# Kernel optimization log

Hardware: AMD Instinct MI355X
Metric: run time of the kernel (lower is better)

## Reference

```python
import jax, jax.numpy as jnp
import numpy as np

N, E = 100000, 1600000
IN_CH, HID, HEADS, OUT_CH = 128, 32, 2, 40
NEG_SLOPE = 0.2
BN_EPS = 1e-5


def _param(key, shape, scale=0.1):
    return scale * jax.random.normal(key, shape, dtype=jnp.float32)


def setup_inputs() -> dict:
    key = jax.random.key(0)
    ks = jax.random.split(key, 24)
    x = jax.random.normal(ks[0], (N, IN_CH), dtype=jnp.float32)
    edge_index = jax.random.randint(ks[1], (2, E), 0, N, dtype=jnp.int32)
    d0 = HEADS * HID  # 64
    inp = {
        'x': x, 'edge_index': edge_index,
        # conv0: in 128 -> 32 per head, concat -> 64
        'W0': _param(ks[2], (IN_CH, HEADS * HID)),
        'as0': _param(ks[3], (HEADS, HID)), 'ad0': _param(ks[4], (HEADS, HID)),
        'b0': jnp.zeros((d0,), jnp.float32),
        'g0': jnp.ones((d0,), jnp.float32), 'bt0': jnp.zeros((d0,), jnp.float32),
        # conv1: 64 -> 32 per head, concat -> 64
        'W1': _param(ks[5], (d0, HEADS * HID)),
        'as1': _param(ks[6], (HEADS, HID)), 'ad1': _param(ks[7], (HEADS, HID)),
        'b1': jnp.zeros((d0,), jnp.float32),
        'g1': jnp.ones((d0,), jnp.float32), 'bt1': jnp.zeros((d0,), jnp.float32),
        # conv2: 64 -> 40 per head, mean over heads -> 40
        'W2': _param(ks[8], (d0, HEADS * OUT_CH)),
        'as2': _param(ks[9], (HEADS, OUT_CH)), 'ad2': _param(ks[10], (HEADS, OUT_CH)),
        'b2': jnp.zeros((OUT_CH,), jnp.float32),
    }
    return inp


def gat_conv(x, src, dst, W, a_src, a_dst, bias, out_ch, concat):
    n = x.shape[0]
    h = (x @ W).reshape(n, HEADS, out_ch)            # [N,H,C]
    alpha_src = jnp.sum(h * a_src, axis=-1)          # [N,H]
    alpha_dst = jnp.sum(h * a_dst, axis=-1)          # [N,H]
    e = jax.nn.leaky_relu(alpha_src[src] + alpha_dst[dst], NEG_SLOPE)  # [E,H]
    # softmax over incoming edges per destination node (self loops guarantee >=1 edge)
    m = jax.ops.segment_max(e, dst, num_segments=n)
    e = jnp.exp(e - m[dst])
    s = jax.ops.segment_sum(e, dst, num_segments=n)
    alpha = e / s[dst]                                # [E,H]
    msg = h[src] * alpha[:, :, None]                  # [E,H,C]
    out = jax.ops.segment_sum(msg, dst, num_segments=n)  # [N,H,C]
    out = out.reshape(n, HEADS * out_ch) if concat else out.mean(axis=1)
    return out + bias


def batch_norm(x, gamma, beta):
    mu = jnp.mean(x, axis=0)
    var = jnp.mean(jnp.square(x - mu), axis=0)
    return gamma * (x - mu) * jax.lax.rsqrt(var + BN_EPS) + beta


def reference(x, edge_index, W0, as0, ad0, b0, g0, bt0,
              W1, as1, ad1, b1, g1, bt1, W2, as2, ad2, b2):
    n = x.shape[0]
    loops = jnp.arange(n, dtype=edge_index.dtype)
    src = jnp.concatenate([edge_index[0], loops])
    dst = jnp.concatenate([edge_index[1], loops])
    h = gat_conv(x, src, dst, W0, as0, ad0, b0, HID, True)
    h = jax.nn.elu(batch_norm(h, g0, bt0))
    h = gat_conv(h, src, dst, W1, as1, ad1, b1, HID, True)
    h = jax.nn.elu(batch_norm(h, g1, bt1))
    return gat_conv(h, src, dst, W2, as2, ad2, b2, OUT_CH, False)
```

## Files before the change

kernel.cpp:

```cpp
#include <hip/hip_runtime.h>
#include <hip/hip_bf16.h>
#include <math.h>


#define NNODES 100000
#define NEDGES 1600000
#define ENTOT  (NEDGES + NNODES)
#define NEG_SLOPE 0.2f
#define BN_EPS 1e-5f

#define NRANGE 8
#define RSIZE  (NNODES/NRANGE)
#define BCAP   262144
#define PBLK   2048
#define NB2    32

typedef unsigned short u16;
typedef unsigned int u32;
typedef unsigned long long u64;
typedef __attribute__((ext_vector_type(8))) short short8;
typedef __attribute__((ext_vector_type(4))) float f32x4;

__device__ __forceinline__ float b2f(u16 u){ union{u32 i; float f;} v; v.i=((u32)u)<<16; return v.f; }
__device__ __forceinline__ float blo(u32 u){ union{u32 i; float f;} v; v.i=u<<16; return v.f; }
__device__ __forceinline__ float bhi(u32 u){ union{u32 i; float f;} v; v.i=u&0xffff0000u; return v.f; }
__device__ __forceinline__ u16 f2b(float x){ __hip_bfloat16 b=__float2bfloat16(x); return *(u16*)&b; }
__device__ __forceinline__ float ldf(const void* p, int i, int f){
  return f ? ((const float*)p)[i] : b2f(((const u16*)p)[i]);
}

__global__ void k_detect(const u16* __restrict__ x, int* __restrict__ flag){
  __shared__ int bad;
  if(threadIdx.x==0) bad=0;
  __syncthreads();
  int cnt=0;
  for(int i=threadIdx.x;i<4096;i+=256){
    u16 v = x[2*i];
    int ex = (v>>7)&0xff;
    if(ex==0xff || (ex==0 && (v&0x7fff)!=0)) cnt++;
  }
  atomicAdd(&bad,cnt);
  __syncthreads();
  if(threadIdx.x==0) flag[0] = (bad>4)?1:0;
}

__global__ __launch_bounds__(256) void k_part2(
    const int* __restrict__ ei, int* __restrict__ gptr, u32* __restrict__ bkt){
  __shared__ int lcnt[NRANGE], gbase[NRANGE];
  int t=threadIdx.x;
  if(t<NRANGE) lcnt[t]=0;
  __syncthreads();
  const int CH=(ENTOT+PBLK-1)/PBLK;
  int beg=blockIdx.x*CH, end=beg+CH; if(end>ENTOT) end=ENTOT;
  int nd[4], ns[4], nr[4], ne=0;
  for(int i=beg+t; i<end; i+=256){
    int d=(i<NEDGES)? ei[NEDGES+i] : (i-NEDGES);
    int s=(i<NEDGES)? ei[i] : d;
    nd[ne]=d; ns[ne]=s; ne++;
  }
  #pragma unroll 4
  for(int k=0;k<ne;k++) nr[k]=atomicAdd(&lcnt[nd[k]/RSIZE],1);
  __syncthreads();
  if(t<NRANGE) gbase[t]=atomicAdd(&gptr[t],lcnt[t]);
  __syncthreads();
  #pragma unroll 4
  for(int k=0;k<ne;k++){
    int r=nd[k]/RSIZE;
    u32 e = ((u32)(nd[k]-r*RSIZE)<<17) | (u32)ns[k];
    __builtin_nontemporal_store(e, &bkt[(size_t)r*BCAP + gbase[r] + nr[k]]);
  }
}

__global__ __launch_bounds__(256) void k_hist4(
    const u32* __restrict__ bkt, const int* __restrict__ gptr, int* __restrict__ lhist){
  __shared__ int lh[RSIZE];
  int t=threadIdx.x;
  for(int i=t;i<RSIZE;i+=256) lh[i]=0;
  __syncthreads();
  int r = blockIdx.x & (NRANGE-1);
  int c = blockIdx.x >> 3;
  int n = gptr[r];
  int per=(n+NB2-1)/NB2;
  int beg=c*per, end=beg+per; if(end>n) end=n;
  const u32* bp = bkt + (size_t)r*BCAP;
  for(int i=beg+t;i<end;i+=256) atomicAdd(&lh[bp[i]>>17],1);
  __syncthreads();
  int* out = lhist + (size_t)(r*NB2+c)*RSIZE;
  for(int i=t;i<RSIZE;i+=256) out[i]=lh[i];
}

__global__ __launch_bounds__(256) void k_sumscan(int* __restrict__ lhist, int* __restrict__ cnt){
  int n = blockIdx.x*256 + threadIdx.x;
  if(n>=NNODES) return;
  int r = n/RSIZE, i = n - r*RSIZE;
  int* base = lhist + (size_t)r*NB2*RSIZE + i;
  int run=0;
  #pragma unroll 8
  for(int c=0;c<NB2;c++){
    int v = base[(size_t)c*RSIZE];
    base[(size_t)c*RSIZE] = run;
    run += v;
  }
  cnt[n]=run;
}

#define SCAN_M (NNODES+1)
#define SCAN_NB ((SCAN_M + 2047)/2048)

__global__ void k_scan_a(const int* __restrict__ cnt, int* __restrict__ bsum){
  __shared__ int red[256];
  int b=blockIdx.x, t=threadIdx.x;
  int base = b*2048 + t*8;
  int s=0;
  #pragma unroll
  for(int j=0;j<8;j++){ int idx=base+j; s += (idx<NNODES)? cnt[idx]:0; }
  red[t]=s; __syncthreads();
  for(int o=128;o>0;o>>=1){ if(t<o) red[t]+=red[t+o]; __syncthreads(); }
  if(t==0) bsum[b]=red[0];
}

__global__ void k_scan_b(int* bsum){
  if(threadIdx.x==0){
    int run=0;
    for(int i=0;i<SCAN_NB;i++){ int v=bsum[i]; bsum[i]=run; run+=v; }
  }
}

__global__ void k_scan_c(const int* __restrict__ cnt, const int* __restrict__ bsum,
                         int* __restrict__ row_ptr){
  __shared__ int lds[256];
  int b=blockIdx.x, t=threadIdx.x;
  int base=b*2048+t*8;
  int v[8]; int s=0;
  #pragma unroll
  for(int j=0;j<8;j++){ int idx=base+j; int x=(idx<NNODES)?cnt[idx]:0; v[j]=s; s+=x; }
  lds[t]=s; __syncthreads();
  for(int o=1;o<256;o<<=1){
    int other=0; if(t>=o) other=lds[t-o];
    __syncthreads();
    lds[t]+=other;
    __syncthreads();
  }
  int texcl = lds[t] - s;
  int off0 = bsum[b] + texcl;
  #pragma unroll
  for(int j=0;j<8;j++){ int idx=base+j; if(idx<SCAN_M) row_ptr[idx]=off0+v[j]; }
}

__global__ __launch_bounds__(256) void k_scatter4(
    const u32* __restrict__ bkt, const int* __restrict__ gptr,
    const int* __restrict__ row_ptr, const int* __restrict__ lhist,
    int* __restrict__ col){
  __shared__ int lofs[RSIZE];
  int t=threadIdx.x;
  int r = blockIdx.x & (NRANGE-1);
  int c = blockIdx.x >> 3;
  int lo = r*RSIZE;
  const int* cb = lhist + (size_t)(r*NB2+c)*RSIZE;
  for(int i=t;i<RSIZE;i+=256) lofs[i] = row_ptr[lo+i] + cb[i];
  __syncthreads();
  int n = gptr[r];
  int per=(n+NB2-1)/NB2;
  int beg=c*per, end=beg+per; if(end>n) end=n;
  const u32* bp = bkt + (size_t)r*BCAP;
  for(int i=beg+t;i<end;i+=256){
    u32 e=bp[i];
    int pos=atomicAdd(&lofs[e>>17],1);
    col[pos]=(int)(e & 0x1FFFF);
  }
}

template<int K, int OUTC, int HID, bool XEXT, bool BN>
__global__ __launch_bounds__(256) void k_gemm_mfma(
    const void* __restrict__ xin, const void* __restrict__ W,
    const void* __restrict__ avs, const void* __restrict__ avd,
    const float2* __restrict__ bnab,
    u16* __restrict__ hout, float* __restrict__ asrc, float* __restrict__ adst,
    const int* __restrict__ flagp)
{
  const int f = flagp[0];
  constexpr int KP = K+8;
  constexpr int RS = OUTC+8;
  constexpr int NT = OUTC/16;
  constexpr int KQ = K/32;
  __shared__ __align__(16) u16 WT[OUTC*KP];
  __shared__ __align__(16) u16 HROW[4*16*RS];
  __shared__ float AVb[2*OUTC];
  __shared__ float2 BB[K];
  int t=threadIdx.x;
  const u16* Wu=(const u16*)W; const float* Wf=(const float*)W;
  for(int i8=t*8; i8<K*OUTC; i8+=256*8){
    int k=i8/OUTC, c0=i8-k*OUTC;
    u16 w8[8];
    if(f){
      const float* wp=Wf+i8;
      float4 a=*(const float4*)wp, b=*(const float4*)(wp+4);
      w8[0]=f2b(a.x);w8[1]=f2b(a.y);w8[2]=f2b(a.z);w8[3]=f2b(a.w);
      w8[4]=f2b(b.x);w8[5]=f2b(b.y);w8[6]=f2b(b.z);w8[7]=f2b(b.w);
    } else {
      uint4 q=*(const uint4*)(Wu+i8);
      w8[0]=q.x&0xffff;w8[1]=q.x>>16;w8[2]=q.y&0xffff;w8[3]=q.y>>16;
      w8[4]=q.z&0xffff;w8[5]=q.z>>16;w8[6]=q.w&0xffff;w8[7]=q.w>>16;
    }
    #pragma unroll
    for(int u=0;u<8;u++) WT[(c0+u)*KP + k] = w8[u];
  }
  for(int idx=t; idx<2*OUTC; idx+=256)
    AVb[idx] = (idx<OUTC)? ldf(avs,idx,f) : ldf(avd,idx-OUTC,f);
  if(BN) for(int idx=t; idx<K; idx+=256) BB[idx]=bnab[idx];
  __syncthreads();

  int wv=t>>6, lane=t&63;
  int m=lane&15, quad=lane>>4;
  int grow0 = blockIdx.x*64 + wv*16;
  int growA = grow0 + m;
  bool avalid = growA < NNODES;
  int growC = avalid ? growA : 0;

  f32x4 acc[NT] = {};
  #pragma unroll
  for(int kq=0;kq<KQ;kq++){
    int k0 = kq*32 + quad*8;
    union{ u32 u[4]; short8 s8; } A;
    if(XEXT && f==1){
      const float* xr=(const float*)xin + (size_t)growC*K + k0;
      float4 p=*(const float4*)xr, q=*(const float4*)(xr+4);
      A.u[0]=f2b(p.x)|((u32)f2b(p.y)<<16);
      A.u[1]=f2b(p.z)|((u32)f2b(p.w)<<16);
      A.u[2]=f2b(q.x)|((u32)f2b(q.y)<<16);
      A.u[3]=f2b(q.z)|((u32)f2b(q.w)<<16);
    } else {
      uint4 q=*(const uint4*)((const u16*)xin + (size_t)growC*K + k0);
      A.u[0]=q.x; A.u[1]=q.y; A.u[2]=q.z; A.u[3]=q.w;
    }
    if(BN){
      #pragma unroll
      for(int j=0;j<4;j++){
        float lo=b2f(A.u[j]&0xffff), hi=b2f(A.u[j]>>16);
        float2 c1=BB[k0+2*j], c2=BB[k0+2*j+1];
        lo=c1.x*lo+c1.y; lo = lo>0.f? lo : __expf(lo)-1.f;
        hi=c2.x*hi+c2.y; hi = hi>0.f? hi : __expf(hi)-1.f;
        A.u[j]=f2b(lo)|((u32)f2b(hi)<<16);
      }
    }
    #pragma unroll
    for(int nt=0;nt<NT;nt++){
      union{ uint4 q; short8 s8; } Bf;
      Bf.q = *(const uint4*)&WT[(nt*16+m)*KP + k0];
      acc[nt] = __builtin_amdgcn_mfma_f32_16x16x32_bf16(A.s8, Bf.s8, acc[nt], 0,0,0);
    }
  }
  u16* hr = &HROW[wv*16*RS];
  #pragma unroll
  for(int nt=0;nt<NT;nt++){
    #pragma unroll
    for(int reg=0;reg<4;reg++)
      hr[(quad*4+reg)*RS + nt*16+m] = f2b(acc[nt][reg]);
  }
  __syncthreads();
  {
    int row=lane&15, task=quad, head=task&1, sd=task>>1;
    float p=0.f;
    const u16* hrow=&hr[row*RS + head*HID];
    const float* av=&AVb[sd*OUTC + head*HID];
    #pragma unroll 8
    for(int c=0;c<HID;c++) p += b2f(hrow[c])*av[c];
    int grow=grow0+row;
    if(grow<NNODES){ (sd? adst:asrc)[grow*2+head]=p; }
  }
  {
    constexpr int CH8 = OUTC/8;
    for(int idx=lane; idx<16*CH8; idx+=64){
      int rr=idx/CH8, c8=idx-rr*CH8;
      int grow=grow0+rr;
      if(grow<NNODES)
        *(uint4*)(hout + (size_t)grow*OUTC + c8*8) = *(const uint4*)&hr[rr*RS + c8*8];
    }
  }
}

template<int OUTC, bool FINAL>
__global__ __launch_bounds__(256) void k_aggf(
  const int* __restrict__ row_ptr, const int* __restrict__ col,
  const u16* __restrict__ hin, const float* __restrict__ asrcf,
  const float2* __restrict__ adst2, const void* __restrict__ bias,
  u16* __restrict__ houtb, void* __restrict__ outv, const int* __restrict__ flagp)
{
  const int f = flagp[0];
  __shared__ float vbuf[FINAL?32:1][84];
  int t = threadIdx.x;
  int g  = t>>3;
  int cg = t&7;
  int rr = blockIdx.x & 7, jb = blockIdx.x >> 3;
  int lim = RSIZE - jb*32;
  bool ok = g < lim;
  int d = rr*RSIZE + jb*32 + g;
  int base=0, deg=0;
  float2 adv = make_float2(0.f,0.f);
  if(ok){
    base = row_ptr[d];
    deg  = row_ptr[d+1] - base;
    adv  = adst2[d];
  }
  const int* cp  = col + base;
  const u16* hcg = hin + cg*8;
  float acc[8]={0,0,0,0,0,0,0,0};

  if(!FINAL){
    int ho = (cg>=4)?1:0;
    float aown = ho ? adv.y : adv.x;
    float s=0.f;
    for(int j=0;j<deg;j+=2){
      int c0 = cp[j];
      bool v1 = (j+1)<deg;
      int c1 = cp[v1 ? j+1 : j];
      float sa = asrcf[c0*2+ho];
      float sb = asrcf[c1*2+ho];
      uint4 h0 = *(const uint4*)(hcg + (size_t)c0*OUTC);
      uint4 h1 = *(const uint4*)(hcg + (size_t)c1*OUTC);
      float e0 = sa+aown; e0 = fmaxf(e0, NEG_SLOPE*e0); e0 = fminf(e0,60.f);
      float e1 = sb+aown; e1 = fmaxf(e1, NEG_SLOPE*e1); e1 = fminf(e1,60.f);
      float p0 = __expf(e0), p1 = __expf(e1);
      if(!v1) p1 = 0.f;
      s += p0 + p1;
      acc[0] += p0*blo(h0.x) + p1*blo(h1.x);
      acc[1] += p0*bhi(h0.x) + p1*bhi(h1.x);
      acc[2] += p0*blo(h0.y) + p1*blo(h1.y);
      acc[3] += p0*bhi(h0.y) + p1*bhi(h1.y);
      acc[4] += p0*blo(h0.z) + p1*blo(h1.z);
      acc[5] += p0*bhi(h0.z) + p1*bhi(h1.z);
      acc[6] += p0*blo(h0.w) + p1*blo(h1.w);
      acc[7] += p0*bhi(h0.w) + p1*bhi(h1.w);
    }
    float inv = s>0.f ? 1.f/s : 0.f;
    if(ok){
      u16 o8[8];
      #pragma unroll
      for(int k=0;k<8;k++) o8[k]=f2b(acc[k]*inv + ldf(bias,cg*8+k,f));
      uint4 ov;
      ov.x=(u32)o8[0]|((u32)o8[1]<<16); ov.y=(u32)o8[2]|((u32)o8[3]<<16);
      ov.z=(u32)o8[4]|((u32)o8[5]<<16); ov.w=(u32)o8[6]|((u32)o8[7]<<16);
      *(uint4*)(houtb + (size_t)d*64 + cg*8) = ov;
    }
  } else {
    const float2* asrc2 = (const float2*)asrcf;
    const u16* hxg = hin + 64 + cg*2;
    float accx0=0.f, accx1=0.f;
    float s0=0.f, s1=0.f;
    for(int j=0;j<deg;j+=2){
      int c0 = cp[j];
      bool v1 = (j+1)<deg;
      int c1 = cp[v1 ? j+1 : j];
      float2 sa = asrc2[c0];
      float2 sv = asrc2[c1];
      const u16* hp0 = hcg + (size_t)c0*OUTC;
      const u16* hp1 = hcg + (size_t)c1*OUTC;
      uint4 h0 = *(const uint4*)hp0;
      uint4 h1 = *(const uint4*)hp1;
      float e0 = sa.x+adv.x; e0 = fmaxf(e0, NEG_SLOPE*e0); e0 = fminf(e0,60.f);
      float e1 = sa.y+adv.y; e1 = fmaxf(e1, NEG_SLOPE*e1); e1 = fminf(e1,60.f);
      float p0 = __expf(e0), p1 = __expf(e1);
      float q0 = sv.x+adv.x; q0 = fmaxf(q0, NEG_SLOPE*q0); q0 = fminf(q0,60.f);
      float q1 = sv.y+adv.y; q1 = fmaxf(q1, NEG_SLOPE*q1); q1 = fminf(q1,60.f);
      float r0 = __expf(q0), r1 = __expf(q1);
      if(!v1){ r0=0.f; r1=0.f; }
      s0 += p0 + r0; s1 += p1 + r1;
      float pa = (cg<5)? p0 : p1;
      float pb = (cg<5)? r0 : r1;
      acc[0] += pa*blo(h0.x) + pb*blo(h1.x);
      acc[1] += pa*bhi(h0.x) + pb*bhi(h1.x);
      acc[2] += pa*blo(h0.y) + pb*blo(h1.y);
      acc[3] += pa*bhi(h0.y) + pb*bhi(h1.y);
      acc[4] += pa*blo(h0.z) + pb*blo(h1.z);
      acc[5] += pa*bhi(h0.z) + pb*bhi(h1.z);
      acc[6] += pa*blo(h0.w) + pb*blo(h1.w);
      acc[7] += pa*bhi(h0.w) + pb*bhi(h1.w);
      ushort2 ha = *(const ushort2*)(hxg + (size_t)c0*OUTC);
      ushort2 hb = *(const ushort2*)(hxg + (size_t)c1*OUTC);
      accx0 += p1*b2f(ha.x) + r1*b2f(hb.x);
      accx1 += p1*b2f(ha.y) + r1*b2f(hb.y);
    }
    float inv0 = s0>0.f?1.f/s0:0.f, inv1 = s1>0.f?1.f/s1:0.f;
    if(ok){
      #pragma unroll
      for(int k=0;k<8;k++)
        vbuf[g][cg*8+k] = acc[k]*((cg<5)?inv0:inv1);
      vbuf[g][64+cg*2]   = accx0*inv1;
      vbuf[g][64+cg*2+1] = accx1*inv1;
    }
    __syncthreads();
    for(int idx=t; idx<32*40; idx+=256){
      int gg=idx/40, ch=idx-gg*40;
      if(gg<lim){
        int dd = rr*RSIZE + jb*32 + gg;
        float res = 0.5f*(vbuf[gg][ch] + vbuf[gg][40+ch]) + ldf(bias,ch,f);
        if(f) ((float*)outv)[(size_t)dd*40+ch] = res;
        else  ((__hip_bfloat16*)outv)[(size_t)dd*40+ch] = __float2bfloat16(res);
      }
    }
  }
}

__global__ __launch_bounds__(256) void k_bnstats(const u16* __restrict__ h, float* __restrict__ stats){
  __shared__ float red[4][128];
  int t=threadIdx.x; int c=t&63; int g=t>>6;
  float s=0.f,q=0.f;
  for(int r=blockIdx.x*4+g; r<NNODES; r+=gridDim.x*4){
    float v=b2f(h[(size_t)r*64+c]); s+=v; q+=v*v;
  }
  red[g][c]=s; red[g][64+c]=q;
  __syncthreads();
  if(t<128){
    float tot=red[0][t]+red[1][t]+red[2][t]+red[3][t];
    atomicAdd(&stats[t], tot);
  }
}

__global__ void k_bnfinal(const float* __restrict__ stats,
                          const void* __restrict__ gm, const void* __restrict__ bt,
                          float2* __restrict__ bnab, const int* __restrict__ flagp){
  const int f = flagp[0];
  int c=threadIdx.x;
  if(c>=64) return;
  float mu=stats[c]*(1.0f/NNODES);
  float var=stats[64+c]*(1.0f/NNODES)-mu*mu;
  var = var>0.f?var:0.f;
  float A = ldf(gm,c,f)*rsqrtf(var+BN_EPS);
  float B = ldf(bt,c,f) - A*mu;
  bnab[c]=make_float2(A,B);
}

extern "C" void kernel_launch(void* const* d_in, const int* in_sizes, int n_in,
                              void* d_out, int out_size, void* d_ws, size_t ws_size,
                              hipStream_t stream){
  const void* x  =d_in[0];
  const int* ei =(const int*)d_in[1];
  const void* W0 =d_in[2];  const void* as0=d_in[3];  const void* ad0=d_in[4];
  const void* b0 =d_in[5];  const void* g0 =d_in[6];  const void* bt0=d_in[7];
  const void* W1 =d_in[8];  const void* as1=d_in[9];  const void* ad1=d_in[10];
  const void* b1 =d_in[11]; const void* g1 =d_in[12]; const void* bt1=d_in[13];
  const void* W2 =d_in[14]; const void* as2=d_in[15]; const void* ad2=d_in[16];
  const void* b2 =d_in[17];

  char* ws=(char*)d_ws;
  size_t off=0;
  auto alloc=[&](size_t bytes)->void*{ void* p=ws+off; off+=(bytes+255)&~(size_t)255; return p; };
  int*    flag   =(int*)   alloc(256);
  int*    row_ptr=(int*)   alloc((size_t)(NNODES+1)*4);
  int*    cnt    =(int*)   alloc((size_t)NNODES*4);
  int*    colx   =(int*)   alloc((size_t)ENTOT*4);
  int*    bsum   =(int*)   alloc((size_t)SCAN_NB*4);
  int*    gptr   =(int*)   alloc(256);
  u32*    bkt    =(u32*)   alloc((size_t)NRANGE*BCAP*4);
  u16*    hA     =(u16*)   alloc((size_t)100032*80*2);
  u16*    hB0    =(u16*)   alloc((size_t)100032*64*2);
  u16*    hB1    =(u16*)   alloc((size_t)100032*64*2);
  float*  asrc   =(float*) alloc((size_t)NNODES*2*4);
  float*  adst   =(float*) alloc((size_t)NNODES*2*4);
  float*  stats  =(float*) alloc(128*4);
  float2* bnab   =(float2*)alloc(64*8);
  int*    lhist  =(int*)hA;

  k_detect<<<1,256,0,stream>>>((const u16*)x, flag);

  (void)hipMemsetAsync(gptr,0,256,stream);
  k_part2  <<<PBLK,256,0,stream>>>(ei,gptr,bkt);
  k_hist4  <<<NRANGE*NB2,256,0,stream>>>(bkt,gptr,lhist);
  k_sumscan<<<(NNODES+255)/256,256,0,stream>>>(lhist,cnt);
  k_scan_a <<<SCAN_NB,256,0,stream>>>(cnt,bsum);
  k_scan_b <<<1,64,0,stream>>>(bsum);
  k_scan_c <<<SCAN_NB,256,0,stream>>>(cnt,bsum,row_ptr);
  k_scatter4<<<NRANGE*NB2,256,0,stream>>>(bkt,gptr,row_ptr,lhist,colx);

  int gG = (NNODES+63)/64;
  int gA = NRANGE * ((RSIZE + 31)/32);
  k_gemm_mfma<128,64,32,true ,false><<<gG,256,0,stream>>>(
      x,W0,as0,ad0,nullptr,hA,asrc,adst,flag);
  k_aggf<64,false><<<gA,256,0,stream>>>(row_ptr,colx,hA,
      asrc,(const float2*)adst,b0,hB0,nullptr,flag);
  (void)hipMemsetAsync(stats,0,512,stream);
  k_bnstats<<<256,256,0,stream>>>(hB0,stats);
  k_bnfinal<<<1,64,0,stream>>>(stats,g0,bt0,bnab,flag);
  k_gemm_mfma<64,64,32,false,true ><<<gG,256,0,stream>>>(
      hB0,W1,as1,ad1,bnab,hA,asrc,adst,flag);
  k_aggf<64,false><<<gA,256,0,stream>>>(row_ptr,colx,hA,
      asrc,(const float2*)adst,b1,hB1,nullptr,flag);
  (void)hipMemsetAsync(stats,0,512,stream);
  k_bnstats<<<256,256,0,stream>>>(hB1,stats);
  k_bnfinal<<<1,64,0,stream>>>(stats,g1,bt1,bnab,flag);
  k_gemm_mfma<64,80,40,false,true ><<<gG,256,0,stream>>>(
      hB1,W2,as2,ad2,bnab,hA,asrc,adst,flag);
  k_aggf<80,true ><<<gA,256,0,stream>>>(row_ptr,colx,hA,
      asrc,(const float2*)adst,b2,nullptr,d_out,flag);

  (void)in_sizes;(void)n_in;(void)out_size;(void)ws_size;
}
```

Baseline: 447.1 us.

## Bucket edges by source range and add phased block sync in aggregation

CSR construction now splits edges into buckets keyed by both destination range and source sub-band, with a local LDS sort before writing each bucket. Within each destination, columns then come out grouped by source band, which should improve cache locality of the gathers in aggregation. The aggregation loops are also cut into four phases with a __syncthreads between them, so warps in a block walk through source bands together and reuse L2. The cost is extra LDS work and scans in partitioning, plus block barriers that can stall warps on high-degree rows. Bucket capacity is now fixed at 24576 entries, which holds only for roughly uniform random graphs.

```diff
diff --git a/kernel.cpp b/kernel.cpp
--- a/kernel.cpp
+++ b/kernel.cpp
@@ -11,11 +11,16 @@
 
 #define NRANGE 8
 #define RSIZE  (NNODES/NRANGE)
-#define BCAP   262144
-#define PBLK   2048
-#define NB2    32
+#define SB     16
+#define SBS    (NNODES/SB)
+#define NBKT   (SB*NRANGE)
+#define BCAP   24576
+#define PBLK2  512
+#define CH2    ((ENTOT+PBLK2-1)/PBLK2)
+#define CHP    3328
 
 typedef unsigned short u16;
+typedef unsigned char u8;
 typedef unsigned int u32;
 typedef unsigned long long u64;
 typedef __attribute__((ext_vector_type(8))) short short8;
@@ -44,30 +49,55 @@
   if(threadIdx.x==0) flag[0] = (bad>4)?1:0;
 }
 
-__global__ __launch_bounds__(256) void k_part2(
+__global__ __launch_bounds__(256) void k_part3(
     const int* __restrict__ ei, int* __restrict__ gptr, u32* __restrict__ bkt){
-  __shared__ int lcnt[NRANGE], gbase[NRANGE];
+  __shared__ u32 ent[CHP];
+  __shared__ u8  bb8[CHP];
+  __shared__ u32 lout[CHP];
+  __shared__ int lcnt[NBKT], lbase[NBKT], gbase[NBKT], lofs[NBKT], stmp[NBKT];
   int t=threadIdx.x;
-  if(t<NRANGE) lcnt[t]=0;
-  __syncthreads();
-  const int CH=(ENTOT+PBLK-1)/PBLK;
-  int beg=blockIdx.x*CH, end=beg+CH; if(end>ENTOT) end=ENTOT;
-  int nd[4], ns[4], nr[4], ne=0;
-  for(int i=beg+t; i<end; i+=256){
-    int d=(i<NEDGES)? ei[NEDGES+i] : (i-NEDGES);
-    int s=(i<NEDGES)? ei[i] : d;
-    nd[ne]=d; ns[ne]=s; ne++;
-  }
-  #pragma unroll 4
-  for(int k=0;k<ne;k++) nr[k]=atomicAdd(&lcnt[nd[k]/RSIZE],1);
-  __syncthreads();
-  if(t<NRANGE) gbase[t]=atomicAdd(&gptr[t],lcnt[t]);
-  __syncthreads();
-  #pragma unroll 4
-  for(int k=0;k<ne;k++){
-    int r=nd[k]/RSIZE;
-    u32 e = ((u32)(nd[k]-r*RSIZE)<<17) | (u32)ns[k];
-    __builtin_nontemporal_store(e, &bkt[(size_t)r*BCAP + gbase[r] + nr[k]]);
+  for(int i=t;i<NBKT;i+=256) lcnt[i]=0;
+  __syncthreads();
+  int beg=blockIdx.x*CH2, end=beg+CH2; if(end>ENTOT) end=ENTOT;
+  int n = end-beg;
+  for(int i=t;i<n;i+=256){
+    int gi = beg+i;
+    int d=(gi<NEDGES)? ei[NEDGES+gi] : (gi-NEDGES);
+    int s=(gi<NEDGES)? ei[gi] : d;
+    int r=d/RSIZE;
+    int b=(s/SBS)*NRANGE + r;
+    ent[i]=((u32)(d-r*RSIZE)<<17)|(u32)s;
+    bb8[i]=(u8)b;
+    atomicAdd(&lcnt[b],1);
+  }
+  __syncthreads();
+  if(t<NBKT) stmp[t]=lcnt[t];
+  __syncthreads();
+  for(int o=1;o<NBKT;o<<=1){
+    int v=(t<NBKT && t>=o)? stmp[t-o]:0;
+    __syncthreads();
+    if(t<NBKT) stmp[t]+=v;
+    __syncthreads();
+  }
+  if(t<NBKT){
+    lbase[t]=stmp[t]-lcnt[t];
+    lofs[t]=stmp[t]-lcnt[t];
+    gbase[t]=atomicAdd(&gptr[t],lcnt[t]);
+  }
+  __syncthreads();
+  for(int i=t;i<n;i+=256){
+    int b=bb8[i];
+    int pos=atomicAdd(&lofs[b],1);
+    lout[pos]=ent[i];
+  }
+  __syncthreads();
+  int wv=t>>6, ln=t&63;
+  for(int b=wv;b<NBKT;b+=4){
+    int lo=lbase[b];
+    int len=((b+1<NBKT)? lbase[b+1] : n) - lo;
+    u32* gdst = bkt + (size_t)b*BCAP + gbase[b];
+    for(int i=ln;i<len;i+=64)
+      __builtin_nontemporal_store(lout[lo+i], &gdst[i]);
   }
 }
 
@@ -77,15 +107,12 @@
   int t=threadIdx.x;
   for(int i=t;i<RSIZE;i+=256) lh[i]=0;
   __syncthreads();
-  int r = blockIdx.x & (NRANGE-1);
-  int c = blockIdx.x >> 3;
-  int n = gptr[r];
-  int per=(n+NB2-1)/NB2;
-  int beg=c*per, end=beg+per; if(end>n) end=n;
-  const u32* bp = bkt + (size_t)r*BCAP;
-  for(int i=beg+t;i<end;i+=256) atomicAdd(&lh[bp[i]>>17],1);
-  __syncthreads();
-  int* out = lhist + (size_t)(r*NB2+c)*RSIZE;
+  int b = blockIdx.x;
+  int n = gptr[b];
+  const u32* bp = bkt + (size_t)b*BCAP;
+  for(int i=t;i<n;i+=256) atomicAdd(&lh[bp[i]>>17],1);
+  __syncthreads();
+  int* out = lhist + (size_t)b*RSIZE;
   for(int i=t;i<RSIZE;i+=256) out[i]=lh[i];
 }
 
@@ -93,12 +120,12 @@
   int n = blockIdx.x*256 + threadIdx.x;
   if(n>=NNODES) return;
   int r = n/RSIZE, i = n - r*RSIZE;
-  int* base = lhist + (size_t)r*NB2*RSIZE + i;
+  int* base = lhist + (size_t)r*RSIZE + i;
   int run=0;
   #pragma unroll 8
-  for(int c=0;c<NB2;c++){
-    int v = base[(size_t)c*RSIZE];
-    base[(size_t)c*RSIZE] = run;
+  for(int sb=0;sb<SB;sb++){
+    int v = base[(size_t)sb*NRANGE*RSIZE];
+    base[(size_t)sb*NRANGE*RSIZE] = run;
     run += v;
   }
   cnt[n]=run;
@@ -153,17 +180,15 @@
     int* __restrict__ col){
   __shared__ int lofs[RSIZE];
   int t=threadIdx.x;
-  int r = blockIdx.x & (NRANGE-1);
-  int c = blockIdx.x >> 3;
+  int b = blockIdx.x;
+  int r = b & (NRANGE-1);
   int lo = r*RSIZE;
-  const int* cb = lhist + (size_t)(r*NB2+c)*RSIZE;
+  const int* cb = lhist + (size_t)b*RSIZE;
   for(int i=t;i<RSIZE;i+=256) lofs[i] = row_ptr[lo+i] + cb[i];
   __syncthreads();
-  int n = gptr[r];
-  int per=(n+NB2-1)/NB2;
-  int beg=c*per, end=beg+per; if(end>n) end=n;
-  const u32* bp = bkt + (size_t)r*BCAP;
-  for(int i=beg+t;i<end;i+=256){
+  int n = gptr[b];
+  const u32* bp = bkt + (size_t)b*BCAP;
+  for(int i=t;i<n;i+=256){
     u32 e=bp[i];
     int pos=atomicAdd(&lofs[e>>17],1);
     col[pos]=(int)(e & 0x1FFFF);
@@ -310,27 +335,32 @@
     int ho = (cg>=4)?1:0;
     float aown = ho ? adv.y : adv.x;
     float s=0.f;
-    for(int j=0;j<deg;j+=2){
-      int c0 = cp[j];
-      bool v1 = (j+1)<deg;
-      int c1 = cp[v1 ? j+1 : j];
-      float sa = asrcf[c0*2+ho];
-      float sb = asrcf[c1*2+ho];
-      uint4 h0 = *(const uint4*)(hcg + (size_t)c0*OUTC);
-      uint4 h1 = *(const uint4*)(hcg + (size_t)c1*OUTC);
-      float e0 = sa+aown; e0 = fmaxf(e0, NEG_SLOPE*e0); e0 = fminf(e0,60.f);
-      float e1 = sb+aown; e1 = fmaxf(e1, NEG_SLOPE*e1); e1 = fminf(e1,60.f);
-      float p0 = __expf(e0), p1 = __expf(e1);
-      if(!v1) p1 = 0.f;
-      s += p0 + p1;
-      acc[0] += p0*blo(h0.x) + p1*blo(h1.x);
-      acc[1] += p0*bhi(h0.x) + p1*bhi(h1.x);
-      acc[2] += p0*blo(h0.y) + p1*blo(h1.y);
-      acc[3] += p0*bhi(h0.y) + p1*bhi(h1.y);
-      acc[4] += p0*blo(h0.z) + p1*blo(h1.z);
-      acc[5] += p0*bhi(h0.z) + p1*bhi(h1.z);
-      acc[6] += p0*blo(h0.w) + p1*blo(h1.w);
-      acc[7] += p0*bhi(h0.w) + p1*bhi(h1.w);
+    for(int ph=0; ph<4; ++ph){
+      int beg = (deg*ph)>>2;
+      int end = (deg*(ph+1))>>2;
+      for(int j=beg; j<end; j+=2){
+        int c0 = cp[j];
+        bool v1 = (j+1)<end;
+        int c1 = cp[v1 ? j+1 : j];
+        float sa = asrcf[c0*2+ho];
+        float sb = asrcf[c1*2+ho];
+        uint4 h0 = *(const uint4*)(hcg + (size_t)c0*OUTC);
+        uint4 h1 = *(const uint4*)(hcg + (size_t)c1*OUTC);
+        float e0 = sa+aown; e0 = fmaxf(e0, NEG_SLOPE*e0); e0 = fminf(e0,60.f);
+        float e1 = sb+aown; e1 = fmaxf(e1, NEG_SLOPE*e1); e1 = fminf(e1,60.f);
+        float p0 = __expf(e0), p1 = __expf(e1);
+        if(!v1) p1 = 0.f;
+        s += p0 + p1;
+        acc[0] += p0*blo(h0.x) + p1*blo(h1.x);
+        acc[1] += p0*bhi(h0.x) + p1*bhi(h1.x);
+        acc[2] += p0*blo(h0.y) + p1*blo(h1.y);
+        acc[3] += p0*bhi(h0.y) + p1*bhi(h1.y);
+        acc[4] += p0*blo(h0.z) + p1*blo(h1.z);
+        acc[5] += p0*bhi(h0.z) + p1*bhi(h1.z);
+        acc[6] += p0*blo(h0.w) + p1*blo(h1.w);
+        acc[7] += p0*bhi(h0.w) + p1*bhi(h1.w);
+      }
+      __syncthreads();
     }
     float inv = s>0.f ? 1.f/s : 0.f;
     if(ok){
@@ -347,38 +377,43 @@
     const u16* hxg = hin + 64 + cg*2;
     float accx0=0.f, accx1=0.f;
     float s0=0.f, s1=0.f;
-    for(int j=0;j<deg;j+=2){
-      int c0 = cp[j];
-      bool v1 = (j+1)<deg;
-      int c1 = cp[v1 ? j+1 : j];
-      float2 sa = asrc2[c0];
-      float2 sv = asrc2[c1];
-      const u16* hp0 = hcg + (size_t)c0*OUTC;
-      const u16* hp1 = hcg + (size_t)c1*OUTC;
-      uint4 h0 = *(const uint4*)hp0;
-      uint4 h1 = *(const uint4*)hp1;
-      float e0 = sa.x+adv.x; e0 = fmaxf(e0, NEG_SLOPE*e0); e0 = fminf(e0,60.f);
-      float e1 = sa.y+adv.y; e1 = fmaxf(e1, NEG_SLOPE*e1); e1 = fminf(e1,60.f);
-      float p0 = __expf(e0), p1 = __expf(e1);
-      float q0 = sv.x+adv.x; q0 = fmaxf(q0, NEG_SLOPE*q0); q0 = fminf(q0,60.f);
-      float q1 = sv.y+adv.y; q1 = fmaxf(q1, NEG_SLOPE*q1); q1 = fminf(q1,60.f);
-      float r0 = __expf(q0), r1 = __expf(q1);
-      if(!v1){ r0=0.f; r1=0.f; }
-      s0 += p0 + r0; s1 += p1 + r1;
-      float pa = (cg<5)? p0 : p1;
-      float pb = (cg<5)? r0 : r1;
-      acc[0] += pa*blo(h0.x) + pb*blo(h1.x);
-      acc[1] += pa*bhi(h0.x) + pb*bhi(h1.x);
-      acc[2] += pa*blo(h0.y) + pb*blo(h1.y);
-      acc[3] += pa*bhi(h0.y) + pb*bhi(h1.y);
-      acc[4] += pa*blo(h0.z) + pb*blo(h1.z);
-      acc[5] += pa*bhi(h0.z) + pb*bhi(h1.z);
-      acc[6] += pa*blo(h0.w) + pb*blo(h1.w);
-      acc[7] += pa*bhi(h0.w) + pb*bhi(h1.w);
-      ushort2 ha = *(const ushort2*)(hxg + (size_t)c0*OUTC);
-      ushort2 hb = *(const ushort2*)(hxg + (size_t)c1*OUTC);
-      accx0 += p1*b2f(ha.x) + r1*b2f(hb.x);
-      accx1 += p1*b2f(ha.y) + r1*b2f(hb.y);
+    for(int ph=0; ph<4; ++ph){
+      int beg = (deg*ph)>>2;
+      int end = (deg*(ph+1))>>2;
+      for(int j=beg; j<end; j+=2){
+        int c0 = cp[j];
+        bool v1 = (j+1)<end;
+        int c1 = cp[v1 ? j+1 : j];
+        float2 sa = asrc2[c0];
+        float2 sv = asrc2[c1];
+        const u16* hp0 = hcg + (size_t)c0*OUTC;
+        const u16* hp1 = hcg + (size_t)c1*OUTC;
+        uint4 h0 = *(const uint4*)hp0;
+        uint4 h1 = *(const uint4*)hp1;
+        float e0 = sa.x+adv.x; e0 = fmaxf(e0, NEG_SLOPE*e0); e0 = fminf(e0,60.f);
+        float e1 = sa.y+adv.y; e1 = fmaxf(e1, NEG_SLOPE*e1); e1 = fminf(e1,60.f);
+        float p0 = __expf(e0), p1 = __expf(e1);
+        float q0 = sv.x+adv.x; q0 = fmaxf(q0, NEG_SLOPE*q0); q0 = fminf(q0,60.f);
+        float q1 = sv.y+adv.y; q1 = fmaxf(q1, NEG_SLOPE*q1); q1 = fminf(q1,60.f);
+        float r0 = __expf(q0), r1 = __expf(q1);
+        if(!v1){ r0=0.f; r1=0.f; }
+        s0 += p0 + r0; s1 += p1 + r1;
+        float pa = (cg<5)? p0 : p1;
+        float pb = (cg<5)? r0 : r1;
+        acc[0] += pa*blo(h0.x) + pb*blo(h1.x);
+        acc[1] += pa*bhi(h0.x) + pb*bhi(h1.x);
+        acc[2] += pa*blo(h0.y) + pb*blo(h1.y);
+        acc[3] += pa*bhi(h0.y) + pb*bhi(h1.y);
+        acc[4] += pa*blo(h0.z) + pb*blo(h1.z);
+        acc[5] += pa*bhi(h0.z) + pb*bhi(h1.z);
+        acc[6] += pa*blo(h0.w) + pb*blo(h1.w);
+        acc[7] += pa*bhi(h0.w) + pb*bhi(h1.w);
+        ushort2 ha = *(const ushort2*)(hxg + (size_t)c0*OUTC);
+        ushort2 hb = *(const ushort2*)(hxg + (size_t)c1*OUTC);
+        accx0 += p1*b2f(ha.x) + r1*b2f(hb.x);
+        accx1 += p1*b2f(ha.y) + r1*b2f(hb.y);
+      }
+      __syncthreads();
     }
     float inv0 = s0>0.f?1.f/s0:0.f, inv1 = s1>0.f?1.f/s1:0.f;
     if(ok){
@@ -450,8 +485,8 @@
   int*    cnt    =(int*)   alloc((size_t)NNODES*4);
   int*    colx   =(int*)   alloc((size_t)ENTOT*4);
   int*    bsum   =(int*)   alloc((size_t)SCAN_NB*4);
-  int*    gptr   =(int*)   alloc(256);
-  u32*    bkt    =(u32*)   alloc((size_t)NRANGE*BCAP*4);
+  int*    gptr   =(int*)   alloc(512);
+  u32*    bkt    =(u32*)   alloc((size_t)NBKT*BCAP*4);
   u16*    hA     =(u16*)   alloc((size_t)100032*80*2);
   u16*    hB0    =(u16*)   alloc((size_t)100032*64*2);
   u16*    hB1    =(u16*)   alloc((size_t)100032*64*2);
@@ -463,14 +498,14 @@
 
   k_detect<<<1,256,0,stream>>>((const u16*)x, flag);
 
-  (void)hipMemsetAsync(gptr,0,256,stream);
-  k_part2  <<<PBLK,256,0,stream>>>(ei,gptr,bkt);
-  k_hist4  <<<NRANGE*NB2,256,0,stream>>>(bkt,gptr,lhist);
+  (void)hipMemsetAsync(gptr,0,512,stream);
+  k_part3  <<<PBLK2,256,0,stream>>>(ei,gptr,bkt);
+  k_hist4  <<<NBKT,256,0,stream>>>(bkt,gptr,lhist);
   k_sumscan<<<(NNODES+255)/256,256,0,stream>>>(lhist,cnt);
   k_scan_a <<<SCAN_NB,256,0,stream>>>(cnt,bsum);
   k_scan_b <<<1,64,0,stream>>>(bsum);
   k_scan_c <<<SCAN_NB,256,0,stream>>>(cnt,bsum,row_ptr);
-  k_scatter4<<<NRANGE*NB2,256,0,stream>>>(bkt,gptr,row_ptr,lhist,colx);
+  k_scatter4<<<NBKT,256,0,stream>>>(bkt,gptr,row_ptr,lhist,colx);
 
   int gG = (NNODES+63)/64;
   int gA = NRANGE * ((RSIZE + 31)/32);
```

Result: slower. 468.7 us (+4.8%).
